# Optimization experiments

Measured on AMD Instinct MI355X. Metric: run time of the kernel, lower is better.

## Reference

```python
import jax, jax.numpy as jnp
import numpy as np

NR = 512      # num robots
NT = 1024     # num tasks
E = 500000    # num edges
D = 64        # robot_dim == task_dim (forced by torch.cat dim=0)
ED = 32       # edge_dim
GH = 128      # gnn_hidden
MH = 128      # mlp_hidden
SLOPE = 0.1   # LeakyReLU negative slope


def lrelu(x):
    return jnp.where(x >= 0, x, SLOPE * x)


def _linear(key, out_d, in_d):
    k1, k2 = jax.random.split(key)
    s = 1.0 / np.sqrt(in_d)
    W = jax.random.uniform(k1, (out_d, in_d), minval=-s, maxval=s, dtype=jnp.float32)
    b = jax.random.uniform(k2, (out_d,), minval=-s, maxval=s, dtype=jnp.float32)
    return W, b


def setup_inputs() -> dict:
    key = jax.random.key(0)
    ks = jax.random.split(key, 12)
    x_robot = jax.random.normal(ks[0], (NR, D), dtype=jnp.float32)
    x_task = jax.random.normal(ks[1], (NT, D), dtype=jnp.float32)
    edge_attr = jax.random.normal(ks[2], (E, ED), dtype=jnp.float32)
    src = jax.random.randint(ks[3], (E,), 0, NR)
    tgt = jax.random.randint(ks[4], (E,), 0, NT)
    edge_index = jnp.stack([src, tgt], axis=0).astype(jnp.int64)
    We1, be1 = _linear(ks[5], GH, 2 * D + ED)   # f_theta_e layer 1
    We2, be2 = _linear(ks[6], GH, GH)            # f_theta_e layer 2
    Wv1, bv1 = _linear(ks[7], GH, D + GH)        # f_theta_v layer 1
    Wv2, bv2 = _linear(ks[8], GH, GH)            # f_theta_v layer 2
    Wm1, bm1 = _linear(ks[9], MH, GH + D)        # task selector layer 1
    Wm2, bm2 = _linear(ks[10], 1, MH)            # task selector layer 2
    return {
        'x_robot': x_robot, 'x_task': x_task, 'edge_index': edge_index,
        'edge_attr': edge_attr,
        'We1': We1, 'be1': be1, 'We2': We2, 'be2': be2,
        'Wv1': Wv1, 'bv1': bv1, 'Wv2': Wv2, 'bv2': bv2,
        'Wm1': Wm1, 'bm1': bm1, 'Wm2': Wm2, 'bm2': bm2,
    }


def reference(x_robot, x_task, edge_index, edge_attr,
              We1, be1, We2, be2, Wv1, bv1, Wv2, bv2, Wm1, bm1, Wm2, bm2):
    n_robot = x_robot.shape[0]
    x = jnp.concatenate([x_robot, x_task], axis=0)          # [NR+NT, D]
    src = edge_index[0]                                      # robot indices
    tgt = edge_index[1] + n_robot                            # shifted task indices
    # PyG default flow='source_to_target': x_i = x[target], x_j = x[source],
    # messages are scatter-added at target slots (the task slots here).
    msg_in = jnp.concatenate([x[tgt], x[src], edge_attr], axis=1)  # [E, 2D+ED]
    m = lrelu(msg_in @ We1.T + be1) @ We2.T + be2            # [E, GH]
    agg = jax.ops.segment_sum(m, tgt, num_segments=n_robot + x_task.shape[0])
    robot_msgs = agg[:n_robot]                               # all zeros (faithful to source)
    upd_in = jnp.concatenate([robot_msgs, x_robot], axis=1)  # [NR, GH+D]
    h = lrelu(upd_in @ Wv1.T + bv1) @ Wv2.T + bv2            # [NR, GH]
    # Pairwise MLP on concat([h_i, task_j]) without materializing the concat:
    # split Wm1 columns into the robot-hidden and task parts.
    hr = h @ Wm1[:, :GH].T                                   # [NR, MH]
    ht = x_task @ Wm1[:, GH:].T                              # [NT, MH]
    hid = lrelu(hr[:, None, :] + ht[None, :, :] + bm1)       # [NR, NT, MH]
    scores = jnp.einsum('nmh,h->nm', hid, Wm2[0]) + bm2[0]   # [NR, NT]
    return jax.nn.softmax(scores, axis=1)
```

## Files before the change

### kernel.cpp

```cpp
#include <hip/hip_runtime.h>

#define NRB 512
#define NTK 1024
#define DD  64
#define GHH 128



__global__ __launch_bounds__(128) void prep_kernel(
    const float* __restrict__ xr, const float* __restrict__ xt,
    const float* __restrict__ Wv1, const float* __restrict__ bv1,
    const float* __restrict__ Wv2, const float* __restrict__ bv2,
    const float* __restrict__ Wm1, const float* __restrict__ bm1,
    const float* __restrict__ Wm2, const float* __restrict__ bm2,
    float* __restrict__ HR, float* __restrict__ HTBt,
    float* __restrict__ av, float* __restrict__ cv, float* __restrict__ wbv)
{
    const int i = threadIdx.x;
    __shared__ float xs[4][DD];
    __shared__ float sA[4][GHH];
    __shared__ float sB[4][GHH];
    __shared__ float sR[4][GHH];
    __shared__ float sT[4][GHH + 1];

    if (blockIdx.x < NRB / 4) {
        const int r0 = blockIdx.x * 4;
        ((float*)xs)[i]       = xr[r0 * DD + i];
        ((float*)xs)[128 + i] = xr[r0 * DD + 128 + i];
        __syncthreads();

        {
            float4 w[16];
            const float4* wp = reinterpret_cast<const float4*>(Wv1 + i * 192 + 128);
            #pragma unroll
            for (int q = 0; q < 16; ++q) w[q] = wp[q];
            const float b = bv1[i];
            for (int r = 0; r < 4; ++r) {
                float acc = b;
                #pragma unroll
                for (int q = 0; q < 16; ++q) {
                    acc = fmaf(w[q].x, xs[r][q*4+0], acc);
                    acc = fmaf(w[q].y, xs[r][q*4+1], acc);
                    acc = fmaf(w[q].z, xs[r][q*4+2], acc);
                    acc = fmaf(w[q].w, xs[r][q*4+3], acc);
                }
                sA[r][i] = (acc >= 0.f) ? acc : 0.1f * acc;
            }
        }
        __syncthreads();

        {
            float4 w[32];
            const float4* wp = reinterpret_cast<const float4*>(Wv2 + i * GHH);
            #pragma unroll
            for (int q = 0; q < 32; ++q) w[q] = wp[q];
            const float b = bv2[i];
            for (int r = 0; r < 4; ++r) {
                float acc = b;
                const float4* hp = reinterpret_cast<const float4*>(sA[r]);
                #pragma unroll
                for (int q = 0; q < 32; ++q) {
                    float4 h4 = hp[q];
                    acc = fmaf(w[q].x, h4.x, acc);
                    acc = fmaf(w[q].y, h4.y, acc);
                    acc = fmaf(w[q].z, h4.z, acc);
                    acc = fmaf(w[q].w, h4.w, acc);
                }
                sB[r][i] = acc;
            }
        }
        __syncthreads();

        {
            float4 w[32];
            const float4* wp = reinterpret_cast<const float4*>(Wm1 + i * 192);
            #pragma unroll
            for (int q = 0; q < 32; ++q) w[q] = wp[q];
            const float wm2 = Wm2[i];
            for (int r = 0; r < 4; ++r) {
                float acc = 0.f;
                const float4* hp = reinterpret_cast<const float4*>(sB[r]);
                #pragma unroll
                for (int q = 0; q < 32; ++q) {
                    float4 h4 = hp[q];
                    acc = fmaf(w[q].x, h4.x, acc);
                    acc = fmaf(w[q].y, h4.y, acc);
                    acc = fmaf(w[q].z, h4.z, acc);
                    acc = fmaf(w[q].w, h4.w, acc);
                }
                HR[(r0 + r) * GHH + i] = acc;
                sR[r][i] = wm2 * acc;
            }
        }
        __syncthreads();
        {
            const int r = i >> 5, c = i & 31;
            float s = sR[r][c] + sR[r][c+32] + sR[r][c+64] + sR[r][c+96];
            #pragma unroll
            for (int off = 16; off >= 1; off >>= 1) s += __shfl_xor(s, off, 32);
            if (c == 0) av[r0 + r] = 0.55f * s;
        }
    } else {
        const int t0 = (blockIdx.x - NRB / 4) * 4;
        ((float*)xs)[i]       = xt[t0 * DD + i];
        ((float*)xs)[128 + i] = xt[t0 * DD + 128 + i];
        __syncthreads();

        float4 w[16];
        const float4* wp = reinterpret_cast<const float4*>(Wm1 + i * 192 + 128);
        #pragma unroll
        for (int q = 0; q < 16; ++q) w[q] = wp[q];
        const float b   = bm1[i];
        const float wm2 = Wm2[i];
        for (int t = 0; t < 4; ++t) {
            float acc = b;
            #pragma unroll
            for (int q = 0; q < 16; ++q) {
                acc = fmaf(w[q].x, xs[t][q*4+0], acc);
                acc = fmaf(w[q].y, xs[t][q*4+1], acc);
                acc = fmaf(w[q].z, xs[t][q*4+2], acc);
                acc = fmaf(w[q].w, xs[t][q*4+3], acc);
            }
            sT[t][i]  = acc;
            sR[t][i]  = wm2 * acc;
        }
        __syncthreads();

        #pragma unroll
        for (int k = 0; k < 4; ++k) {
            const int wdx = i + k * 128;
            const int h   = wdx >> 2;
            const int m   = wdx & 3;
            HTBt[h * NTK + t0 + m] = sT[m][h];
        }
        {
            const int r = i >> 5, c = i & 31;
            float s = sR[r][c] + sR[r][c+32] + sR[r][c+64] + sR[r][c+96];
            #pragma unroll
            for (int off = 16; off >= 1; off >>= 1) s += __shfl_xor(s, off, 32);
            if (c == 0) cv[t0 + r] = 0.55f * s + bm2[0];
        }
        if (blockIdx.x == NRB / 4) wbv[i] = 0.45f * wm2;
    }
}

__global__ __launch_bounds__(1024) void score_softmax_kernel(
    const float* __restrict__ HR, const float* __restrict__ HTBt,
    const float* __restrict__ av, const float* __restrict__ cv,
    const float* __restrict__ wbv, float* __restrict__ out)
{
    const int b   = blockIdx.x;
    const int tid = threadIdx.x;
    const int n0  = b * 2;

    const float* hr0 = HR + n0 * GHH;
    const float* hr1 = hr0 + GHH;
    const float* tbp = HTBt + tid;

    float acc0 = 0.f, acc1 = 0.f;

    #pragma unroll 8
    for (int h = 0; h < 128; ++h) {
        const float tb = tbp[h * NTK];
        const float w  = wbv[h];
        const float r0 = hr0[h];
        const float r1 = hr1[h];
        acc0 = fmaf(w, fabsf(r0 + tb), acc0);
        acc1 = fmaf(w, fabsf(r1 + tb), acc1);
    }

    const float cm = cv[tid];
    float sc[2];
    sc[0] = acc0 + av[n0]     + cm;
    sc[1] = acc1 + av[n0 + 1] + cm;

    __shared__ float rmax[2][16], rsum[2][16];
    const int wid = tid >> 6, lane = tid & 63;

    #pragma unroll
    for (int n = 0; n < 2; ++n) {
        float mx = sc[n];
        #pragma unroll
        for (int off = 32; off >= 1; off >>= 1)
            mx = fmaxf(mx, __shfl_xor(mx, off, 64));
        if (lane == 0) rmax[n][wid] = mx;
    }
    __syncthreads();

    float ex[2];
    #pragma unroll
    for (int n = 0; n < 2; ++n) {
        float mx = rmax[n][0];
        #pragma unroll
        for (int k = 1; k < 16; ++k) mx = fmaxf(mx, rmax[n][k]);
        float e = expf(sc[n] - mx);
        ex[n] = e;
        float s = e;
        #pragma unroll
        for (int off = 32; off >= 1; off >>= 1) s += __shfl_xor(s, off, 64);
        if (lane == 0) rsum[n][wid] = s;
    }
    __syncthreads();

    #pragma unroll
    for (int n = 0; n < 2; ++n) {
        float s = rsum[n][0];
        #pragma unroll
        for (int k = 1; k < 16; ++k) s += rsum[n][k];
        out[(n0 + n) * NTK + tid] = ex[n] * (1.0f / s);
    }
}

extern "C" void kernel_launch(void* const* d_in, const int* in_sizes, int n_in,
                              void* d_out, int out_size, void* d_ws, size_t ws_size,
                              hipStream_t stream)
{
    const float* xr  = (const float*)d_in[0];
    const float* xt  = (const float*)d_in[1];
    const float* Wv1 = (const float*)d_in[8];
    const float* bv1 = (const float*)d_in[9];
    const float* Wv2 = (const float*)d_in[10];
    const float* bv2 = (const float*)d_in[11];
    const float* Wm1 = (const float*)d_in[12];
    const float* bm1 = (const float*)d_in[13];
    const float* Wm2 = (const float*)d_in[14];
    const float* bm2 = (const float*)d_in[15];

    float* ws   = (float*)d_ws;
    float* HR   = ws;
    float* HTBt = ws + 65536;
    float* av   = ws + 196608;
    float* cv   = ws + 197120;
    float* wbv  = ws + 198144;
    float* out  = (float*)d_out;

    hipLaunchKernelGGL(prep_kernel, dim3(384), dim3(128), 0, stream,
                       xr, xt, Wv1, bv1, Wv2, bv2, Wm1, bm1, Wm2, bm2,
                       HR, HTBt, av, cv, wbv);
    hipLaunchKernelGGL(score_softmax_kernel, dim3(256), dim3(1024), 0, stream,
                       HR, HTBt, av, cv, wbv, out);
}
```

Before: 26.06 us.

## Stage transposed weights in LDS for prep and cache per-row vectors in score kernel

The prep kernel now runs 256-thread blocks. Each block cooperatively loads the weight matrices into LDS, transposed and padded, instead of having every thread hold a whole weight row in registers. Task blocks handle 8 tasks each, which cuts the grid from 384 to 256 blocks and lowers register pressure. The score kernel stages the two HR rows and wbv into shared memory, replacing repeated global loads in its loop. In exchange, the block adds a ~66KB LDS footprint and extra barriers, which may limit occupancy.

Measured after the change: 27.16 us. +4.2%, slower.

```diff
diff --git a/kernel.cpp b/kernel.cpp
--- a/kernel.cpp
+++ b/kernel.cpp
@@ -7,7 +7,7 @@
 
 
 
-__global__ __launch_bounds__(128) void prep_kernel(
+__global__ __launch_bounds__(256) void prep_kernel(
     const float* __restrict__ xr, const float* __restrict__ xt,
     const float* __restrict__ Wv1, const float* __restrict__ bv1,
     const float* __restrict__ Wv2, const float* __restrict__ bv2,
@@ -16,131 +16,187 @@
     float* __restrict__ HR, float* __restrict__ HTBt,
     float* __restrict__ av, float* __restrict__ cv, float* __restrict__ wbv)
 {
-    const int i = threadIdx.x;
-    __shared__ float xs[4][DD];
-    __shared__ float sA[4][GHH];
-    __shared__ float sB[4][GHH];
-    __shared__ float sR[4][GHH];
-    __shared__ float sT[4][GHH + 1];
-
-    if (blockIdx.x < NRB / 4) {
-        const int r0 = blockIdx.x * 4;
-        ((float*)xs)[i]       = xr[r0 * DD + i];
-        ((float*)xs)[128 + i] = xr[r0 * DD + 128 + i];
-        __syncthreads();
-
-        {
-            float4 w[16];
-            const float4* wp = reinterpret_cast<const float4*>(Wv1 + i * 192 + 128);
-            #pragma unroll
-            for (int q = 0; q < 16; ++q) w[q] = wp[q];
-            const float b = bv1[i];
-            for (int r = 0; r < 4; ++r) {
-                float acc = b;
-                #pragma unroll
-                for (int q = 0; q < 16; ++q) {
-                    acc = fmaf(w[q].x, xs[r][q*4+0], acc);
-                    acc = fmaf(w[q].y, xs[r][q*4+1], acc);
-                    acc = fmaf(w[q].z, xs[r][q*4+2], acc);
-                    acc = fmaf(w[q].w, xs[r][q*4+3], acc);
-                }
-                sA[r][i] = (acc >= 0.f) ? acc : 0.1f * acc;
-            }
-        }
-        __syncthreads();
-
-        {
-            float4 w[32];
-            const float4* wp = reinterpret_cast<const float4*>(Wv2 + i * GHH);
-            #pragma unroll
-            for (int q = 0; q < 32; ++q) w[q] = wp[q];
-            const float b = bv2[i];
-            for (int r = 0; r < 4; ++r) {
-                float acc = b;
-                const float4* hp = reinterpret_cast<const float4*>(sA[r]);
-                #pragma unroll
-                for (int q = 0; q < 32; ++q) {
-                    float4 h4 = hp[q];
-                    acc = fmaf(w[q].x, h4.x, acc);
-                    acc = fmaf(w[q].y, h4.y, acc);
-                    acc = fmaf(w[q].z, h4.z, acc);
-                    acc = fmaf(w[q].w, h4.w, acc);
-                }
-                sB[r][i] = acc;
-            }
-        }
-        __syncthreads();
-
-        {
-            float4 w[32];
-            const float4* wp = reinterpret_cast<const float4*>(Wm1 + i * 192);
-            #pragma unroll
-            for (int q = 0; q < 32; ++q) w[q] = wp[q];
+    const int t = threadIdx.x;
+    const int b = blockIdx.x;
+    const int i = t & 127;
+    const int g = t >> 7;
+
+    __shared__ float lds_w[128 * 129];
+    __shared__ float xs[8][64];
+    __shared__ float sA[4][128];
+    __shared__ float sB[4][128];
+    __shared__ float sT[8][132];
+    __shared__ float sR[8][132];
+
+    if (b < 128) {
+        const int r0 = b * 4;
+        ((float*)xs)[t] = xr[r0 * DD + t];
+
+        {
+            const float4* W = reinterpret_cast<const float4*>(Wv1);
+            #pragma unroll
+            for (int j = 0; j < 8; ++j) {
+                const int e   = t + 256 * j;
+                const int row = e >> 4, c4 = e & 15;
+                float4 v = W[row * 48 + 32 + c4];
+                const int k0 = c4 * 4;
+                lds_w[(k0+0)*129 + row] = v.x;
+                lds_w[(k0+1)*129 + row] = v.y;
+                lds_w[(k0+2)*129 + row] = v.z;
+                lds_w[(k0+3)*129 + row] = v.w;
+            }
+        }
+        __syncthreads();
+
+        {
+            float a0 = bv1[i], a1 = a0;
+            const float* x0 = xs[2*g];
+            const float* x1 = xs[2*g + 1];
+            #pragma unroll 8
+            for (int k = 0; k < 64; ++k) {
+                const float w = lds_w[k*129 + i];
+                a0 = fmaf(w, x0[k], a0);
+                a1 = fmaf(w, x1[k], a1);
+            }
+            sA[2*g][i]     = (a0 >= 0.f) ? a0 : 0.1f * a0;
+            sA[2*g + 1][i] = (a1 >= 0.f) ? a1 : 0.1f * a1;
+        }
+        __syncthreads();
+
+        {
+            const float4* W = reinterpret_cast<const float4*>(Wv2);
+            #pragma unroll
+            for (int j = 0; j < 16; ++j) {
+                const int e   = t + 256 * j;
+                const int row = e >> 5, c4 = e & 31;
+                float4 v = W[row * 32 + c4];
+                const int k0 = c4 * 4;
+                lds_w[(k0+0)*129 + row] = v.x;
+                lds_w[(k0+1)*129 + row] = v.y;
+                lds_w[(k0+2)*129 + row] = v.z;
+                lds_w[(k0+3)*129 + row] = v.w;
+            }
+        }
+        __syncthreads();
+
+        {
+            float a0 = bv2[i], a1 = a0;
+            const float* h0 = sA[2*g];
+            const float* h1 = sA[2*g + 1];
+            #pragma unroll 8
+            for (int k = 0; k < 128; ++k) {
+                const float w = lds_w[k*129 + i];
+                a0 = fmaf(w, h0[k], a0);
+                a1 = fmaf(w, h1[k], a1);
+            }
+            sB[2*g][i]     = a0;
+            sB[2*g + 1][i] = a1;
+        }
+        __syncthreads();
+
+        {
+            const float4* W = reinterpret_cast<const float4*>(Wm1);
+            #pragma unroll
+            for (int j = 0; j < 16; ++j) {
+                const int e   = t + 256 * j;
+                const int row = e >> 5, c4 = e & 31;
+                float4 v = W[row * 48 + c4];
+                const int k0 = c4 * 4;
+                lds_w[(k0+0)*129 + row] = v.x;
+                lds_w[(k0+1)*129 + row] = v.y;
+                lds_w[(k0+2)*129 + row] = v.z;
+                lds_w[(k0+3)*129 + row] = v.w;
+            }
+        }
+        __syncthreads();
+
+        {
             const float wm2 = Wm2[i];
-            for (int r = 0; r < 4; ++r) {
-                float acc = 0.f;
-                const float4* hp = reinterpret_cast<const float4*>(sB[r]);
-                #pragma unroll
-                for (int q = 0; q < 32; ++q) {
-                    float4 h4 = hp[q];
-                    acc = fmaf(w[q].x, h4.x, acc);
-                    acc = fmaf(w[q].y, h4.y, acc);
-                    acc = fmaf(w[q].z, h4.z, acc);
-                    acc = fmaf(w[q].w, h4.w, acc);
-                }
-                HR[(r0 + r) * GHH + i] = acc;
-                sR[r][i] = wm2 * acc;
-            }
-        }
-        __syncthreads();
-        {
-            const int r = i >> 5, c = i & 31;
-            float s = sR[r][c] + sR[r][c+32] + sR[r][c+64] + sR[r][c+96];
-            #pragma unroll
-            for (int off = 16; off >= 1; off >>= 1) s += __shfl_xor(s, off, 32);
-            if (c == 0) av[r0 + r] = 0.55f * s;
+            float a0 = 0.f, a1 = 0.f;
+            const float* h0 = sB[2*g];
+            const float* h1 = sB[2*g + 1];
+            #pragma unroll 8
+            for (int k = 0; k < 128; ++k) {
+                const float w = lds_w[k*129 + i];
+                a0 = fmaf(w, h0[k], a0);
+                a1 = fmaf(w, h1[k], a1);
+            }
+            HR[(r0 + 2*g) * GHH + i]     = a0;
+            HR[(r0 + 2*g + 1) * GHH + i] = a1;
+            sR[2*g][i]     = wm2 * a0;
+            sR[2*g + 1][i] = wm2 * a1;
+        }
+        __syncthreads();
+
+        {
+            const int row = t >> 6, c = t & 63;
+            float s = sR[row][c] + sR[row][c + 64];
+            #pragma unroll
+            for (int off = 32; off >= 1; off >>= 1)
+                s += __shfl_xor(s, off, 64);
+            if (c == 0) av[r0 + row] = 0.55f * s;
         }
     } else {
-        const int t0 = (blockIdx.x - NRB / 4) * 4;
-        ((float*)xs)[i]       = xt[t0 * DD + i];
-        ((float*)xs)[128 + i] = xt[t0 * DD + 128 + i];
-        __syncthreads();
-
-        float4 w[16];
-        const float4* wp = reinterpret_cast<const float4*>(Wm1 + i * 192 + 128);
-        #pragma unroll
-        for (int q = 0; q < 16; ++q) w[q] = wp[q];
-        const float b   = bm1[i];
-        const float wm2 = Wm2[i];
-        for (int t = 0; t < 4; ++t) {
-            float acc = b;
-            #pragma unroll
-            for (int q = 0; q < 16; ++q) {
-                acc = fmaf(w[q].x, xs[t][q*4+0], acc);
-                acc = fmaf(w[q].y, xs[t][q*4+1], acc);
-                acc = fmaf(w[q].z, xs[t][q*4+2], acc);
-                acc = fmaf(w[q].w, xs[t][q*4+3], acc);
-            }
-            sT[t][i]  = acc;
-            sR[t][i]  = wm2 * acc;
-        }
-        __syncthreads();
-
-        #pragma unroll
-        for (int k = 0; k < 4; ++k) {
-            const int wdx = i + k * 128;
-            const int h   = wdx >> 2;
-            const int m   = wdx & 3;
-            HTBt[h * NTK + t0 + m] = sT[m][h];
-        }
-        {
-            const int r = i >> 5, c = i & 31;
-            float s = sR[r][c] + sR[r][c+32] + sR[r][c+64] + sR[r][c+96];
-            #pragma unroll
-            for (int off = 16; off >= 1; off >>= 1) s += __shfl_xor(s, off, 32);
-            if (c == 0) cv[t0 + r] = 0.55f * s + bm2[0];
-        }
-        if (blockIdx.x == NRB / 4) wbv[i] = 0.45f * wm2;
+        const int t0 = (b - 128) * 8;
+        ((float*)xs)[t]       = xt[t0 * DD + t];
+        ((float*)xs)[256 + t] = xt[t0 * DD + 256 + t];
+
+        {
+            const float4* W = reinterpret_cast<const float4*>(Wm1);
+            #pragma unroll
+            for (int j = 0; j < 8; ++j) {
+                const int e   = t + 256 * j;
+                const int row = e >> 4, c4 = e & 15;
+                float4 v = W[row * 48 + 32 + c4];
+                const int k0 = c4 * 4;
+                lds_w[(k0+0)*129 + row] = v.x;
+                lds_w[(k0+1)*129 + row] = v.y;
+                lds_w[(k0+2)*129 + row] = v.z;
+                lds_w[(k0+3)*129 + row] = v.w;
+            }
+        }
+        __syncthreads();
+
+        {
+            const float bb  = bm1[i];
+            const float wm2 = Wm2[i];
+            float a0 = bb, a1 = bb, a2 = bb, a3 = bb;
+            const float* x0 = xs[4*g];
+            const float* x1 = xs[4*g + 1];
+            const float* x2 = xs[4*g + 2];
+            const float* x3 = xs[4*g + 3];
+            #pragma unroll 8
+            for (int k = 0; k < 64; ++k) {
+                const float w = lds_w[k*129 + i];
+                a0 = fmaf(w, x0[k], a0);
+                a1 = fmaf(w, x1[k], a1);
+                a2 = fmaf(w, x2[k], a2);
+                a3 = fmaf(w, x3[k], a3);
+            }
+            sT[4*g][i]     = a0;  sR[4*g][i]     = wm2 * a0;
+            sT[4*g + 1][i] = a1;  sR[4*g + 1][i] = wm2 * a1;
+            sT[4*g + 2][i] = a2;  sR[4*g + 2][i] = wm2 * a2;
+            sT[4*g + 3][i] = a3;  sR[4*g + 3][i] = wm2 * a3;
+        }
+        __syncthreads();
+
+        #pragma unroll
+        for (int j = 0; j < 4; ++j) {
+            const int e  = t + 256 * j;
+            const int h  = e >> 3, tk = e & 7;
+            HTBt[h * NTK + t0 + tk] = sT[tk][h];
+        }
+
+        {
+            const int row = t >> 5, c = t & 31;
+            float s = sR[row][c] + sR[row][c + 32]
+                    + sR[row][c + 64] + sR[row][c + 96];
+            #pragma unroll
+            for (int off = 16; off >= 1; off >>= 1)
+                s += __shfl_xor(s, off, 32);
+            if (c == 0) cv[t0 + row] = 0.55f * s + bm2[0];
+        }
+        if (b == 128 && t < GHH) wbv[t] = 0.45f * Wm2[t];
     }
 }
 
@@ -153,20 +209,21 @@
     const int tid = threadIdx.x;
     const int n0  = b * 2;
 
-    const float* hr0 = HR + n0 * GHH;
-    const float* hr1 = hr0 + GHH;
+    __shared__ float s_hr[2 * GHH];
+    __shared__ float s_wb[GHH];
+    if (tid < 256)      s_hr[tid]       = HR[n0 * GHH + tid];
+    else if (tid < 384) s_wb[tid - 256] = wbv[tid - 256];
+    __syncthreads();
+
     const float* tbp = HTBt + tid;
-
     float acc0 = 0.f, acc1 = 0.f;
 
     #pragma unroll 8
     for (int h = 0; h < 128; ++h) {
         const float tb = tbp[h * NTK];
-        const float w  = wbv[h];
-        const float r0 = hr0[h];
-        const float r1 = hr1[h];
-        acc0 = fmaf(w, fabsf(r0 + tb), acc0);
-        acc1 = fmaf(w, fabsf(r1 + tb), acc1);
+        const float w  = s_wb[h];
+        acc0 = fmaf(w, fabsf(s_hr[h] + tb), acc0);
+        acc1 = fmaf(w, fabsf(s_hr[GHH + h] + tb), acc1);
     }
 
     const float cm = cv[tid];
@@ -234,7 +291,7 @@
     float* wbv  = ws + 198144;
     float* out  = (float*)d_out;
 
-    hipLaunchKernelGGL(prep_kernel, dim3(384), dim3(128), 0, stream,
+    hipLaunchKernelGGL(prep_kernel, dim3(256), dim3(256), 0, stream,
                        xr, xt, Wv1, bv1, Wv2, bv2, Wm1, bm1, Wm2, bm2,
                        HR, HTBt, av, cv, wbv);
     hipLaunchKernelGGL(score_softmax_kernel, dim3(256), dim3(1024), 0, stream,
```
